# Performance work log

Measured on AMD Instinct MI355X. Metric: run time of the kernel, lower is better.

Reference implementation:

```python
import jax, jax.numpy as jnp
import numpy as np
from jax import lax

B, T = 64, 512
VOCAB, EMBED, UNITS = 32000, 256, 512


def setup_inputs() -> dict:
    key = jax.random.key(0)
    ks = jax.random.split(key, 8)
    s = 0.05
    G = 4 * UNITS
    return {
        "encoder_input": jax.random.randint(ks[0], (B, T), 0, VOCAB, dtype=jnp.int32),
        "embedding": jax.random.normal(ks[1], (VOCAB, EMBED), jnp.float32) * s,
        "W_fwd": jax.random.normal(ks[2], (EMBED, G), jnp.float32) * s,
        "U_fwd": jax.random.normal(ks[3], (UNITS, G), jnp.float32) * s,
        "b_fwd": jnp.zeros((G,), jnp.float32),
        "W_bwd": jax.random.normal(ks[4], (EMBED, G), jnp.float32) * s,
        "U_bwd": jax.random.normal(ks[5], (UNITS, G), jnp.float32) * s,
        "b_bwd": jnp.zeros((G,), jnp.float32),
    }


def _lstm_scan(x, mask, W, Uw, b, reverse):
    """Masked LSTM over time. Keras semantics: at masked steps the (h, c)
    state is carried through unchanged and the emitted output repeats the
    previous hidden state (which for LSTM equals the carried h).
    x: [B, T, E] float, mask: [B, T] bool."""
    Bsz = x.shape[0]
    Uh = Uw.shape[0]
    # Precompute input projection for all timesteps: [B, T, 4U]
    xz = jnp.einsum("bte,eg->btg", x, W) + b

    def step(carry, inp):
        h, c = carry
        z_x, m = inp  # z_x: [B, 4U], m: [B]
        z = z_x + h @ Uw
        i, f, g, o = jnp.split(z, 4, axis=-1)  # Keras gate order i, f, c, o
        i = jax.nn.sigmoid(i)
        f = jax.nn.sigmoid(f)
        g = jnp.tanh(g)
        o = jax.nn.sigmoid(o)
        c_new = f * c + i * g
        h_new = o * jnp.tanh(c_new)
        m = m[:, None]
        h = jnp.where(m, h_new, h)
        c = jnp.where(m, c_new, c)
        return (h, c), h

    h0 = jnp.zeros((Bsz, Uh), x.dtype)
    c0 = jnp.zeros((Bsz, Uh), x.dtype)
    (h, c), ys = lax.scan(
        step, (h0, c0), (xz.swapaxes(0, 1), mask.T), reverse=reverse
    )
    # lax.scan with reverse=True stacks outputs in original time order,
    # matching Keras Bidirectional's reverse-then-re-reverse behavior.
    return ys.swapaxes(0, 1), h, c


def reference(encoder_input, embedding, W_fwd, U_fwd, b_fwd, W_bwd, U_bwd, b_bwd):
    mask = encoder_input != 0  # mask_zero=True
    emb = embedding[encoder_input]  # [B, T, E]
    out_f, h_f, c_f = _lstm_scan(emb, mask, W_fwd, U_fwd, b_fwd, reverse=False)
    out_b, h_b, c_b = _lstm_scan(emb, mask, W_bwd, U_bwd, b_bwd, reverse=True)
    encoder_output = jnp.concatenate([out_f, out_b], axis=-1)  # [B, T, 2U]
    final_state_h = jnp.concatenate([h_f, h_b], axis=-1)  # [B, 2U]
    final_state_c = jnp.concatenate([c_f, c_b], axis=-1)  # [B, 2U]
    # Dropout is identity at inference (training=False default).
    return encoder_output, final_state_h, final_state_c
```

## Files before the change

kernel.cpp:

```cpp
#include <hip/hip_runtime.h>
#include <cstdint>


#define B_ 64
#define T_ 512
#define E_ 256

typedef __attribute__((ext_vector_type(8))) short bf16x8;
typedef __attribute__((ext_vector_type(4))) float f32x4;

__device__ __forceinline__ unsigned short f2bf(float x) {
  unsigned u = __float_as_uint(x);
  u += 0x7FFFu + ((u >> 16) & 1u);
  return (unsigned short)(u >> 16);
}
__device__ __forceinline__ float sigm(float x) { return 1.0f / (1.0f + __expf(-x)); }
__device__ __forceinline__ float tanh_(float x) { return 1.0f - 2.0f / (__expf(2.0f * x) + 1.0f); }

__global__ void prep_kernel(const int* __restrict__ enc, const float* __restrict__ emb,
                            unsigned short* __restrict__ o) {
  const int bi = blockIdx.x;
  const int t = bi >> 6, b = bi & 63;
  const int tok = enc[b * T_ + t];
  float4 v = ((const float4*)(emb + (size_t)tok * E_))[threadIdx.x];
  ushort4 w;
  w.x = f2bf(v.x); w.y = f2bf(v.y); w.z = f2bf(v.z); w.w = f2bf(v.w);
  ((ushort4*)(o + (size_t)t * (B_ * E_) + b * E_))[threadIdx.x] = w;
}

__global__ __launch_bounds__(256, 1)
void lstm_kernel(const int* __restrict__ enc, const unsigned short* __restrict__ embq,
                 const float* __restrict__ Wf, const float* __restrict__ Uf, const float* __restrict__ bfv,
                 const float* __restrict__ Wb, const float* __restrict__ Ub, const float* __restrict__ bbv,
                 unsigned short* __restrict__ Hbuf, unsigned* __restrict__ cnt,
                 float* __restrict__ out) {
  const int tid = threadIdx.x;
  const int lane = tid & 63;
  const int wave = tid >> 6;
  const int mh = wave & 1, nh = wave >> 1;
  const int l15 = lane & 15, l4 = lane >> 4;
  const int d = blockIdx.x >> 5;
  const int cg = blockIdx.x & 31;
  const int u0 = cg * 16;
  const float* Wd = d ? Wb : Wf;
  const float* Ud = d ? Ub : Uf;
  const float* bd = d ? bbv : bfv;

  __shared__ float Z[64][68];

  bf16x8 u_frag[16][2];
#pragma unroll
  for (int ks = 0; ks < 16; ++ks) {
#pragma unroll
    for (int ns = 0; ns < 2; ++ns) {
      const int gate = nh * 2 + ns;
      const int col = gate * 512 + u0 + l15;
      const int k0 = ks * 32 + l4 * 8;
      bf16x8 f;
#pragma unroll
      for (int i = 0; i < 8; ++i) f[i] = (short)f2bf(Ud[(size_t)(k0 + i) * 2048 + col]);
      u_frag[ks][ns] = f;
    }
  }
  bf16x8 w_frag[8][2];
#pragma unroll
  for (int ks = 0; ks < 8; ++ks) {
#pragma unroll
    for (int ns = 0; ns < 2; ++ns) {
      const int gate = nh * 2 + ns;
      const int col = gate * 512 + u0 + l15;
      const int k0 = ks * 32 + l4 * 8;
      bf16x8 f;
#pragma unroll
      for (int i = 0; i < 8; ++i) f[i] = (short)f2bf(Wd[(size_t)(k0 + i) * 2048 + col]);
      w_frag[ks][ns] = f;
    }
  }

  const int ej = tid & 15;
  const int ebg = tid >> 4;
  float bias[4];
#pragma unroll
  for (int g = 0; g < 4; ++g) bias[g] = bd[g * 512 + u0 + ej];

  float hst[4] = {0.f, 0.f, 0.f, 0.f}, cst[4] = {0.f, 0.f, 0.f, 0.f};

  bf16x8 apf[8][2];
  int mpf[4];
  {
    const int t0 = d ? 511 : 0;
    const unsigned short* eT = embq + (size_t)t0 * (B_ * E_);
#pragma unroll
    for (int ks = 0; ks < 8; ++ks)
#pragma unroll
      for (int ms = 0; ms < 2; ++ms) {
        const int b = mh * 32 + ms * 16 + l15;
        const int e0 = ks * 32 + l4 * 8;
        apf[ks][ms] = *(const bf16x8*)(eT + b * E_ + e0);
      }
#pragma unroll
    for (int r = 0; r < 4; ++r) mpf[r] = enc[(ebg * 4 + r) * T_ + t0];
  }

  unsigned* cntd = cnt + d * 513;

  for (int s = 0; s < 512; ++s) {
    const int t = d ? (511 - s) : s;
    f32x4 acc[2][2];
#pragma unroll
    for (int ms = 0; ms < 2; ++ms)
#pragma unroll
      for (int ns = 0; ns < 2; ++ns) acc[ms][ns] = (f32x4)0.0f;

#pragma unroll
    for (int ks = 0; ks < 8; ++ks)
#pragma unroll
      for (int ms = 0; ms < 2; ++ms)
#pragma unroll
        for (int ns = 0; ns < 2; ++ns)
          acc[ms][ns] = __builtin_amdgcn_mfma_f32_16x16x32_bf16(apf[ks][ms], w_frag[ks][ns],
                                                                acc[ms][ns], 0, 0, 0);

    if (s > 0) {
      if (tid == 0) {
        while (__hip_atomic_load(cntd + s, __ATOMIC_RELAXED, __HIP_MEMORY_SCOPE_AGENT) < 32u) {}
      }
      __syncthreads();

      bf16x8 ha[16][2];
      {
        const unsigned short* Hrd = Hbuf + ((size_t)((s & 1) * 2 + d)) * 32768;
        const char* lb = (const char*)Hrd + (l4 >> 1) * 2048 + mh * 1024 + l15 * 32 + (l4 & 1) * 16;
        const char* b0p = lb + 0 * 8192 + 4096;
        const char* b1p = lb + 1 * 8192 + 4096;
        const char* b2p = lb + 2 * 8192 + 4096;
        const char* b3p = lb + 3 * 8192 + 4096;
        const char* b4p = lb + 4 * 8192 + 4096;
        const char* b5p = lb + 5 * 8192 + 4096;
        const char* b6p = lb + 6 * 8192 + 4096;
        const char* b7p = lb + 7 * 8192 + 4096;
        asm volatile(
          "global_load_dwordx4 %0, %32, off offset:-4096 sc0 sc1\n\t"
          "global_load_dwordx4 %1, %32, off offset:-3584 sc0 sc1\n\t"
          "global_load_dwordx4 %2, %32, off offset:0 sc0 sc1\n\t"
          "global_load_dwordx4 %3, %32, off offset:512 sc0 sc1\n\t"
          "global_load_dwordx4 %4, %33, off offset:-4096 sc0 sc1\n\t"
          "global_load_dwordx4 %5, %33, off offset:-3584 sc0 sc1\n\t"
          "global_load_dwordx4 %6, %33, off offset:0 sc0 sc1\n\t"
          "global_load_dwordx4 %7, %33, off offset:512 sc0 sc1\n\t"
          "global_load_dwordx4 %8, %34, off offset:-4096 sc0 sc1\n\t"
          "global_load_dwordx4 %9, %34, off offset:-3584 sc0 sc1\n\t"
          "global_load_dwordx4 %10, %34, off offset:0 sc0 sc1\n\t"
          "global_load_dwordx4 %11, %34, off offset:512 sc0 sc1\n\t"
          "global_load_dwordx4 %12, %35, off offset:-4096 sc0 sc1\n\t"
          "global_load_dwordx4 %13, %35, off offset:-3584 sc0 sc1\n\t"
          "global_load_dwordx4 %14, %35, off offset:0 sc0 sc1\n\t"
          "global_load_dwordx4 %15, %35, off offset:512 sc0 sc1\n\t"
          "global_load_dwordx4 %16, %36, off offset:-4096 sc0 sc1\n\t"
          "global_load_dwordx4 %17, %36, off offset:-3584 sc0 sc1\n\t"
          "global_load_dwordx4 %18, %36, off offset:0 sc0 sc1\n\t"
          "global_load_dwordx4 %19, %36, off offset:512 sc0 sc1\n\t"
          "global_load_dwordx4 %20, %37, off offset:-4096 sc0 sc1\n\t"
          "global_load_dwordx4 %21, %37, off offset:-3584 sc0 sc1\n\t"
          "global_load_dwordx4 %22, %37, off offset:0 sc0 sc1\n\t"
          "global_load_dwordx4 %23, %37, off offset:512 sc0 sc1\n\t"
          "global_load_dwordx4 %24, %38, off offset:-4096 sc0 sc1\n\t"
          "global_load_dwordx4 %25, %38, off offset:-3584 sc0 sc1\n\t"
          "global_load_dwordx4 %26, %38, off offset:0 sc0 sc1\n\t"
          "global_load_dwordx4 %27, %38, off offset:512 sc0 sc1\n\t"
          "global_load_dwordx4 %28, %39, off offset:-4096 sc0 sc1\n\t"
          "global_load_dwordx4 %29, %39, off offset:-3584 sc0 sc1\n\t"
          "global_load_dwordx4 %30, %39, off offset:0 sc0 sc1\n\t"
          "global_load_dwordx4 %31, %39, off offset:512 sc0 sc1\n\t"
          "s_waitcnt vmcnt(0)"
          : "=v"(ha[0][0]), "=v"(ha[0][1]), "=v"(ha[1][0]), "=v"(ha[1][1]),
            "=v"(ha[2][0]), "=v"(ha[2][1]), "=v"(ha[3][0]), "=v"(ha[3][1]),
            "=v"(ha[4][0]), "=v"(ha[4][1]), "=v"(ha[5][0]), "=v"(ha[5][1]),
            "=v"(ha[6][0]), "=v"(ha[6][1]), "=v"(ha[7][0]), "=v"(ha[7][1]),
            "=v"(ha[8][0]), "=v"(ha[8][1]), "=v"(ha[9][0]), "=v"(ha[9][1]),
            "=v"(ha[10][0]), "=v"(ha[10][1]), "=v"(ha[11][0]), "=v"(ha[11][1]),
            "=v"(ha[12][0]), "=v"(ha[12][1]), "=v"(ha[13][0]), "=v"(ha[13][1]),
            "=v"(ha[14][0]), "=v"(ha[14][1]), "=v"(ha[15][0]), "=v"(ha[15][1])
          : "v"(b0p), "v"(b1p), "v"(b2p), "v"(b3p),
            "v"(b4p), "v"(b5p), "v"(b6p), "v"(b7p)
          : "memory");
      }
#pragma unroll
      for (int ks = 0; ks < 16; ++ks) {
        acc[0][0] = __builtin_amdgcn_mfma_f32_16x16x32_bf16(ha[ks][0], u_frag[ks][0], acc[0][0], 0, 0, 0);
        acc[0][1] = __builtin_amdgcn_mfma_f32_16x16x32_bf16(ha[ks][0], u_frag[ks][1], acc[0][1], 0, 0, 0);
        acc[1][0] = __builtin_amdgcn_mfma_f32_16x16x32_bf16(ha[ks][1], u_frag[ks][0], acc[1][0], 0, 0, 0);
        acc[1][1] = __builtin_amdgcn_mfma_f32_16x16x32_bf16(ha[ks][1], u_frag[ks][1], acc[1][1], 0, 0, 0);
      }
    } else {
      __syncthreads();
    }

#pragma unroll
    for (int ms = 0; ms < 2; ++ms)
#pragma unroll
      for (int ns = 0; ns < 2; ++ns)
#pragma unroll
        for (int r = 0; r < 4; ++r)
          Z[mh * 32 + ms * 16 + l4 * 4 + r][nh * 32 + ns * 16 + l15] = acc[ms][ns][r];
    __syncthreads();

    unsigned hu[4];
    {
      const bool last = (s == 511);
#pragma unroll
      for (int r = 0; r < 4; ++r) {
        const int b = ebg * 4 + r;
        float zi = Z[b][ej] + bias[0];
        float zf = Z[b][16 + ej] + bias[1];
        float zg = Z[b][32 + ej] + bias[2];
        float zo = Z[b][48 + ej] + bias[3];
        float ig = sigm(zi), fg = sigm(zf), gg = tanh_(zg), og = sigm(zo);
        float cn = fg * cst[r] + ig * gg;
        float hn = og * tanh_(cn);
        const bool m = (mpf[r] != 0);
        cst[r] = m ? cn : cst[r];
        hst[r] = m ? hn : hst[r];
        hu[r] = (unsigned)f2bf(hst[r]);
        out[((size_t)b * T_ + t) * 1024 + d * 512 + u0 + ej] = hst[r];
        if (last) {
          out[33554432u + (size_t)b * 1024 + d * 512 + u0 + ej] = hst[r];
          out[33619968u + (size_t)b * 1024 + d * 512 + u0 + ej] = cst[r];
        }
      }
    }

    if (s < 511) {
      const int tn = d ? (510 - s) : (s + 1);
      const unsigned short* eT = embq + (size_t)tn * (B_ * E_);
#pragma unroll
      for (int ks = 0; ks < 8; ++ks)
#pragma unroll
        for (int ms = 0; ms < 2; ++ms) {
          const int b = mh * 32 + ms * 16 + l15;
          const int e0 = ks * 32 + l4 * 8;
          apf[ks][ms] = *(const bf16x8*)(eT + b * E_ + e0);
        }
#pragma unroll
      for (int r = 0; r < 4; ++r) mpf[r] = enc[(ebg * 4 + r) * T_ + tn];
    }

    {
      unsigned short* Hwr = Hbuf + ((size_t)(((s + 1) & 1) * 2 + d)) * 32768 + cg * 1024;
      char* hp = (char*)(Hwr + ebg * 64 + ej);
      asm volatile(
        "global_store_short %0, %1, off sc0 sc1\n\t"
        "global_store_short %0, %2, off offset:32 sc0 sc1\n\t"
        "global_store_short %0, %3, off offset:64 sc0 sc1\n\t"
        "global_store_short %0, %4, off offset:96 sc0 sc1\n\t"
        "s_waitcnt vmcnt(0)"
        :: "v"(hp), "v"(hu[0]), "v"(hu[1]), "v"(hu[2]), "v"(hu[3])
        : "memory");
    }
    __syncthreads();
    if (tid == 0)
      __hip_atomic_fetch_add(cntd + (s + 1), 1u, __ATOMIC_RELAXED, __HIP_MEMORY_SCOPE_AGENT);
  }
}

extern "C" void kernel_launch(void* const* d_in, const int* in_sizes, int n_in,
                              void* d_out, int out_size, void* d_ws, size_t ws_size,
                              hipStream_t stream) {
  const int* enc = (const int*)d_in[0];
  const float* emb = (const float*)d_in[1];
  const float* Wf = (const float*)d_in[2];
  const float* Uf = (const float*)d_in[3];
  const float* bf = (const float*)d_in[4];
  const float* Wb = (const float*)d_in[5];
  const float* Ub = (const float*)d_in[6];
  const float* bb = (const float*)d_in[7];
  float* out = (float*)d_out;
  char* ws = (char*)d_ws;

  unsigned short* embq = (unsigned short*)ws;
  unsigned short* Hbuf = (unsigned short*)(ws + (16u << 20));
  unsigned* cnt = (unsigned*)(ws + (16u << 20) + 262144u);

  hipMemsetAsync(ws + (16u << 20) + 262144u, 0, 4104u, stream);
  prep_kernel<<<32768, 64, 0, stream>>>(enc, emb, embq);
  lstm_kernel<<<64, 256, 0, stream>>>(enc, embq, Wf, Uf, bf, Wb, Ub, bb, Hbuf, cnt, out);
}
```

Baseline: 3.426 ms.

## Replace atomic step counter with per-block flags and overlap loads with compute

Each step's counter, which 32 blocks incremented atomically, becomes 32 per-block flag words. Thirty-two threads poll them in parallel, removing atomic contention on the critical path. Several latency-hiding changes come with it. The next step's embedding and mask prefetch moves ahead of the barrier wait, the h-state loads are split so the first half of the MFMAs starts before all loads land, and the output stores are issued after the flag signal. The prep kernel also switches to 256-thread blocks. The costs are a larger flag workspace and more live registers.

```diff
diff --git a/kernel.cpp b/kernel.cpp
--- a/kernel.cpp
+++ b/kernel.cpp
@@ -19,20 +19,22 @@
 
 __global__ void prep_kernel(const int* __restrict__ enc, const float* __restrict__ emb,
                             unsigned short* __restrict__ o) {
-  const int bi = blockIdx.x;
-  const int t = bi >> 6, b = bi & 63;
+  const int g = blockIdx.x * 256 + threadIdx.x;
+  const int e4 = g & 63;
+  const int row = g >> 6;
+  const int b = row & 63, t = row >> 6;
   const int tok = enc[b * T_ + t];
-  float4 v = ((const float4*)(emb + (size_t)tok * E_))[threadIdx.x];
+  float4 v = ((const float4*)(emb + (size_t)tok * E_))[e4];
   ushort4 w;
   w.x = f2bf(v.x); w.y = f2bf(v.y); w.z = f2bf(v.z); w.w = f2bf(v.w);
-  ((ushort4*)(o + (size_t)t * (B_ * E_) + b * E_))[threadIdx.x] = w;
+  ((ushort4*)(o + (size_t)t * (B_ * E_) + b * E_))[e4] = w;
 }
 
 __global__ __launch_bounds__(256, 1)
 void lstm_kernel(const int* __restrict__ enc, const unsigned short* __restrict__ embq,
                  const float* __restrict__ Wf, const float* __restrict__ Uf, const float* __restrict__ bfv,
                  const float* __restrict__ Wb, const float* __restrict__ Ub, const float* __restrict__ bbv,
-                 unsigned short* __restrict__ Hbuf, unsigned* __restrict__ cnt,
+                 unsigned short* __restrict__ Hbuf, unsigned* __restrict__ flags,
                  float* __restrict__ out) {
   const int tid = threadIdx.x;
   const int lane = tid & 63;
@@ -86,7 +88,7 @@
   float hst[4] = {0.f, 0.f, 0.f, 0.f}, cst[4] = {0.f, 0.f, 0.f, 0.f};
 
   bf16x8 apf[8][2];
-  int mpf[4];
+  int mpf[2][4];
   {
     const int t0 = d ? 511 : 0;
     const unsigned short* eT = embq + (size_t)t0 * (B_ * E_);
@@ -99,13 +101,14 @@
         apf[ks][ms] = *(const bf16x8*)(eT + b * E_ + e0);
       }
 #pragma unroll
-    for (int r = 0; r < 4; ++r) mpf[r] = enc[(ebg * 4 + r) * T_ + t0];
+    for (int r = 0; r < 4; ++r) mpf[0][r] = enc[(ebg * 4 + r) * T_ + t0];
   }
 
-  unsigned* cntd = cnt + d * 513;
+  unsigned* flagd = flags + d * 513 * 32;
 
   for (int s = 0; s < 512; ++s) {
     const int t = d ? (511 - s) : s;
+    const int cur = s & 1;
     f32x4 acc[2][2];
 #pragma unroll
     for (int ms = 0; ms < 2; ++ms)
@@ -121,9 +124,25 @@
           acc[ms][ns] = __builtin_amdgcn_mfma_f32_16x16x32_bf16(apf[ks][ms], w_frag[ks][ns],
                                                                 acc[ms][ns], 0, 0, 0);
 
+    if (s < 511) {
+      const int tn = d ? (510 - s) : (s + 1);
+      const unsigned short* eT = embq + (size_t)tn * (B_ * E_);
+#pragma unroll
+      for (int ks = 0; ks < 8; ++ks)
+#pragma unroll
+        for (int ms = 0; ms < 2; ++ms) {
+          const int b = mh * 32 + ms * 16 + l15;
+          const int e0 = ks * 32 + l4 * 8;
+          apf[ks][ms] = *(const bf16x8*)(eT + b * E_ + e0);
+        }
+#pragma unroll
+      for (int r = 0; r < 4; ++r) mpf[cur ^ 1][r] = enc[(ebg * 4 + r) * T_ + tn];
+    }
+
     if (s > 0) {
-      if (tid == 0) {
-        while (__hip_atomic_load(cntd + s, __ATOMIC_RELAXED, __HIP_MEMORY_SCOPE_AGENT) < 32u) {}
+      if (tid < 32) {
+        const unsigned* fp = flagd + s * 32 + tid;
+        while (__hip_atomic_load(fp, __ATOMIC_RELAXED, __HIP_MEMORY_SCOPE_AGENT) == 0u) {}
       }
       __syncthreads();
 
@@ -172,26 +191,38 @@
           "global_load_dwordx4 %29, %39, off offset:-3584 sc0 sc1\n\t"
           "global_load_dwordx4 %30, %39, off offset:0 sc0 sc1\n\t"
           "global_load_dwordx4 %31, %39, off offset:512 sc0 sc1\n\t"
-          "s_waitcnt vmcnt(0)"
-          : "=v"(ha[0][0]), "=v"(ha[0][1]), "=v"(ha[1][0]), "=v"(ha[1][1]),
-            "=v"(ha[2][0]), "=v"(ha[2][1]), "=v"(ha[3][0]), "=v"(ha[3][1]),
-            "=v"(ha[4][0]), "=v"(ha[4][1]), "=v"(ha[5][0]), "=v"(ha[5][1]),
-            "=v"(ha[6][0]), "=v"(ha[6][1]), "=v"(ha[7][0]), "=v"(ha[7][1]),
-            "=v"(ha[8][0]), "=v"(ha[8][1]), "=v"(ha[9][0]), "=v"(ha[9][1]),
-            "=v"(ha[10][0]), "=v"(ha[10][1]), "=v"(ha[11][0]), "=v"(ha[11][1]),
-            "=v"(ha[12][0]), "=v"(ha[12][1]), "=v"(ha[13][0]), "=v"(ha[13][1]),
-            "=v"(ha[14][0]), "=v"(ha[14][1]), "=v"(ha[15][0]), "=v"(ha[15][1])
+          "s_waitcnt vmcnt(16)"
+          : "=&v"(ha[0][0]), "=&v"(ha[0][1]), "=&v"(ha[1][0]), "=&v"(ha[1][1]),
+            "=&v"(ha[2][0]), "=&v"(ha[2][1]), "=&v"(ha[3][0]), "=&v"(ha[3][1]),
+            "=&v"(ha[4][0]), "=&v"(ha[4][1]), "=&v"(ha[5][0]), "=&v"(ha[5][1]),
+            "=&v"(ha[6][0]), "=&v"(ha[6][1]), "=&v"(ha[7][0]), "=&v"(ha[7][1]),
+            "=&v"(ha[8][0]), "=&v"(ha[8][1]), "=&v"(ha[9][0]), "=&v"(ha[9][1]),
+            "=&v"(ha[10][0]), "=&v"(ha[10][1]), "=&v"(ha[11][0]), "=&v"(ha[11][1]),
+            "=&v"(ha[12][0]), "=&v"(ha[12][1]), "=&v"(ha[13][0]), "=&v"(ha[13][1]),
+            "=&v"(ha[14][0]), "=&v"(ha[14][1]), "=&v"(ha[15][0]), "=&v"(ha[15][1])
           : "v"(b0p), "v"(b1p), "v"(b2p), "v"(b3p),
             "v"(b4p), "v"(b5p), "v"(b6p), "v"(b7p)
           : "memory");
       }
 #pragma unroll
-      for (int ks = 0; ks < 16; ++ks) {
+      for (int ks = 0; ks < 8; ++ks) {
         acc[0][0] = __builtin_amdgcn_mfma_f32_16x16x32_bf16(ha[ks][0], u_frag[ks][0], acc[0][0], 0, 0, 0);
         acc[0][1] = __builtin_amdgcn_mfma_f32_16x16x32_bf16(ha[ks][0], u_frag[ks][1], acc[0][1], 0, 0, 0);
         acc[1][0] = __builtin_amdgcn_mfma_f32_16x16x32_bf16(ha[ks][1], u_frag[ks][0], acc[1][0], 0, 0, 0);
         acc[1][1] = __builtin_amdgcn_mfma_f32_16x16x32_bf16(ha[ks][1], u_frag[ks][1], acc[1][1], 0, 0, 0);
       }
+      asm volatile("s_waitcnt vmcnt(0)"
+        : "+v"(ha[8][0]), "+v"(ha[8][1]), "+v"(ha[9][0]), "+v"(ha[9][1]),
+          "+v"(ha[10][0]), "+v"(ha[10][1]), "+v"(ha[11][0]), "+v"(ha[11][1]),
+          "+v"(ha[12][0]), "+v"(ha[12][1]), "+v"(ha[13][0]), "+v"(ha[13][1]),
+          "+v"(ha[14][0]), "+v"(ha[14][1]), "+v"(ha[15][0]), "+v"(ha[15][1]) ::);
+#pragma unroll
+      for (int ks = 8; ks < 16; ++ks) {
+        acc[0][0] = __builtin_amdgcn_mfma_f32_16x16x32_bf16(ha[ks][0], u_frag[ks][0], acc[0][0], 0, 0, 0);
+        acc[0][1] = __builtin_amdgcn_mfma_f32_16x16x32_bf16(ha[ks][0], u_frag[ks][1], acc[0][1], 0, 0, 0);
+        acc[1][0] = __builtin_amdgcn_mfma_f32_16x16x32_bf16(ha[ks][1], u_frag[ks][0], acc[1][0], 0, 0, 0);
+        acc[1][1] = __builtin_amdgcn_mfma_f32_16x16x32_bf16(ha[ks][1], u_frag[ks][1], acc[1][1], 0, 0, 0);
+      }
     } else {
       __syncthreads();
     }
@@ -206,43 +237,19 @@
     __syncthreads();
 
     unsigned hu[4];
-    {
-      const bool last = (s == 511);
-#pragma unroll
-      for (int r = 0; r < 4; ++r) {
-        const int b = ebg * 4 + r;
-        float zi = Z[b][ej] + bias[0];
-        float zf = Z[b][16 + ej] + bias[1];
-        float zg = Z[b][32 + ej] + bias[2];
-        float zo = Z[b][48 + ej] + bias[3];
-        float ig = sigm(zi), fg = sigm(zf), gg = tanh_(zg), og = sigm(zo);
-        float cn = fg * cst[r] + ig * gg;
-        float hn = og * tanh_(cn);
-        const bool m = (mpf[r] != 0);
-        cst[r] = m ? cn : cst[r];
-        hst[r] = m ? hn : hst[r];
-        hu[r] = (unsigned)f2bf(hst[r]);
-        out[((size_t)b * T_ + t) * 1024 + d * 512 + u0 + ej] = hst[r];
-        if (last) {
-          out[33554432u + (size_t)b * 1024 + d * 512 + u0 + ej] = hst[r];
-          out[33619968u + (size_t)b * 1024 + d * 512 + u0 + ej] = cst[r];
-        }
-      }
-    }
-
-    if (s < 511) {
-      const int tn = d ? (510 - s) : (s + 1);
-      const unsigned short* eT = embq + (size_t)tn * (B_ * E_);
-#pragma unroll
-      for (int ks = 0; ks < 8; ++ks)
-#pragma unroll
-        for (int ms = 0; ms < 2; ++ms) {
-          const int b = mh * 32 + ms * 16 + l15;
-          const int e0 = ks * 32 + l4 * 8;
-          apf[ks][ms] = *(const bf16x8*)(eT + b * E_ + e0);
-        }
-#pragma unroll
-      for (int r = 0; r < 4; ++r) mpf[r] = enc[(ebg * 4 + r) * T_ + tn];
+#pragma unroll
+    for (int r = 0; r < 4; ++r) {
+      float zi = Z[ebg * 4 + r][ej] + bias[0];
+      float zf = Z[ebg * 4 + r][16 + ej] + bias[1];
+      float zg = Z[ebg * 4 + r][32 + ej] + bias[2];
+      float zo = Z[ebg * 4 + r][48 + ej] + bias[3];
+      float ig = sigm(zi), fg = sigm(zf), gg = tanh_(zg), og = sigm(zo);
+      float cn = fg * cst[r] + ig * gg;
+      float hn = og * tanh_(cn);
+      const bool m = (mpf[cur][r] != 0);
+      cst[r] = m ? cn : cst[r];
+      hst[r] = m ? hn : hst[r];
+      hu[r] = (unsigned)f2bf(hst[r]);
     }
 
     {
@@ -259,7 +266,20 @@
     }
     __syncthreads();
     if (tid == 0)
-      __hip_atomic_fetch_add(cntd + (s + 1), 1u, __ATOMIC_RELAXED, __HIP_MEMORY_SCOPE_AGENT);
+      __hip_atomic_store(flagd + (s + 1) * 32 + cg, 1u, __ATOMIC_RELAXED, __HIP_MEMORY_SCOPE_AGENT);
+
+    {
+      const bool last = (s == 511);
+#pragma unroll
+      for (int r = 0; r < 4; ++r) {
+        const int b = ebg * 4 + r;
+        out[((size_t)b * T_ + t) * 1024 + d * 512 + u0 + ej] = hst[r];
+        if (last) {
+          out[33554432u + (size_t)b * 1024 + d * 512 + u0 + ej] = hst[r];
+          out[33619968u + (size_t)b * 1024 + d * 512 + u0 + ej] = cst[r];
+        }
+      }
+    }
   }
 }
 
@@ -279,9 +299,9 @@
 
   unsigned short* embq = (unsigned short*)ws;
   unsigned short* Hbuf = (unsigned short*)(ws + (16u << 20));
-  unsigned* cnt = (unsigned*)(ws + (16u << 20) + 262144u);
-
-  hipMemsetAsync(ws + (16u << 20) + 262144u, 0, 4104u, stream);
-  prep_kernel<<<32768, 64, 0, stream>>>(enc, emb, embq);
-  lstm_kernel<<<64, 256, 0, stream>>>(enc, embq, Wf, Uf, bf, Wb, Ub, bb, Hbuf, cnt, out);
+  unsigned* flags = (unsigned*)(ws + (16u << 20) + 262144u);
+
+  hipMemsetAsync(ws + (16u << 20) + 262144u, 0, 131328u, stream);
+  prep_kernel<<<8192, 256, 0, stream>>>(enc, emb, embq);
+  lstm_kernel<<<64, 256, 0, stream>>>(enc, embq, Wf, Uf, bf, Wb, Ub, bb, Hbuf, flags, out);
 }
```

Measured after the change: 3.560 ms. 3.9% more time.
